# Kernel optimization log

Measured on AMD Instinct MI355X. Metric: run time of the kernel, lower is better.

Reference implementation:

```python
import jax, jax.numpy as jnp
import numpy as np

G = 16          # GroupNorm groups
EPS = 1e-5


def setup_inputs() -> dict:
    key = jax.random.key(0)
    ks = jax.random.split(key, 6)
    B, C, H, W = 2, 256, 96, 96
    O = 256
    x = jax.random.normal(ks[0], (B, C, H, W), dtype=jnp.float32)
    offset = jax.random.normal(ks[1], (B, 18, H, W), dtype=jnp.float32)
    mask = jax.random.uniform(ks[2], (B, 9, H, W), dtype=jnp.float32)
    fan_in = C * 9
    weight = jax.random.normal(ks[3], (O, C, 3, 3), dtype=jnp.float32) / np.sqrt(fan_in)
    bias = jnp.zeros((O,), dtype=jnp.float32)
    gamma = jnp.ones((O,), dtype=jnp.float32)
    beta = jnp.zeros((O,), dtype=jnp.float32)
    return {"x": x, "offset": offset, "mask": mask, "weight": weight,
            "bias": bias, "gamma": gamma, "beta": beta}


def _mdcn_gn(x, offset, mask, weight, bias, gamma, beta):
    B, C, H, W = x.shape
    O = weight.shape[0]
    K = 9
    # offsets: mmcv layout [y0,x0,y1,x1,...] per kernel point k = kh*3+kw
    off = offset.reshape(B, K, 2, H, W)
    off_y, off_x = off[:, :, 0], off[:, :, 1]            # [B,K,H,W]
    ky = (jnp.arange(K) // 3 - 1).astype(x.dtype)        # kernel dy, pad=1
    kx = (jnp.arange(K) % 3 - 1).astype(x.dtype)
    hh = jnp.arange(H, dtype=x.dtype)[:, None]
    ww = jnp.arange(W, dtype=x.dtype)[None, :]
    py = hh[None, None] + ky[:, None, None] + off_y      # [B,K,H,W] sample y
    px = ww[None, None] + kx[:, None, None] + off_x      # [B,K,H,W] sample x

    y0 = jnp.floor(py)
    x0 = jnp.floor(px)
    dy = py - y0
    dx = px - x0
    y0i = y0.astype(jnp.int32)
    x0i = x0.astype(jnp.int32)

    xf = x.reshape(B, C, H * W)

    def gather(yi, xi):
        # zero-padded bilinear corner: out-of-range corners contribute 0
        valid = ((yi >= 0) & (yi < H) & (xi >= 0) & (xi < W)).astype(x.dtype)
        yc = jnp.clip(yi, 0, H - 1)
        xc = jnp.clip(xi, 0, W - 1)
        idx = (yc * W + xc).reshape(B, 1, K * H * W)
        v = jnp.take_along_axis(xf, idx, axis=2).reshape(B, C, K, H, W)
        return v * valid.reshape(B, 1, K, H, W)

    w00 = ((1 - dy) * (1 - dx))[:, None]                 # [B,1,K,H,W]
    w01 = ((1 - dy) * dx)[:, None]
    w10 = (dy * (1 - dx))[:, None]
    w11 = (dy * dx)[:, None]
    val = (gather(y0i, x0i) * w00 + gather(y0i, x0i + 1) * w01 +
           gather(y0i + 1, x0i) * w10 + gather(y0i + 1, x0i + 1) * w11)
    val = val * mask[:, None]                            # modulation [B,C,K,H,W]

    out = jnp.einsum('ock,bckhw->bohw', weight.reshape(O, C, K), val)
    out = out + bias[None, :, None, None]

    # GroupNorm(16, O)
    xg = out.reshape(B, G, O // G, H, W)
    mean = xg.mean(axis=(2, 3, 4), keepdims=True)
    var = jnp.mean((xg - mean) ** 2, axis=(2, 3, 4), keepdims=True)
    xn = ((xg - mean) * jax.lax.rsqrt(var + EPS)).reshape(B, O, H, W)
    return xn * gamma[None, :, None, None] + beta[None, :, None, None]


def reference(x, offset, mask, weight, bias, gamma, beta):
    return _mdcn_gn(x, offset, mask, weight, bias, gamma, beta)
```

## Files before the change

### kernel.cpp

```cpp
#include <hip/hip_runtime.h>
#include <hip/hip_fp16.h>

typedef _Float16 f16;
typedef __attribute__((ext_vector_type(2))) _Float16 h2v;
typedef __attribute__((ext_vector_type(8))) _Float16 f16x8;
typedef __attribute__((ext_vector_type(4))) float f32x4;

#define HW_    9216
#define PADP   8
#define XP_    112
#define XPXP_  12544
#define NSTEP  72
#define NMT    288
#define XT_BYTES   12845056
#define BMAT_BYTES 1179648
#define ATILE_B    294912
#define A32_B      147456
#define OUTH_BYTES 9437184
#define PART_BYTES 36864

union U4 { uint4 u; h2v h[4]; f16x8 v; f16 f[8]; };
union U1 { unsigned u; h2v h; };
union UO { ushort4 s; f16 f[4]; };

__global__ __launch_bounds__(256) void k_zero(uint4* __restrict__ p) {
    int i = blockIdx.x*1024 + threadIdx.x;
    uint4 z = {0u,0u,0u,0u};
    p[i] = z; p[i+256] = z; p[i+512] = z; p[i+768] = z;
}

__global__ __launch_bounds__(256) void k_prep_x(const float* __restrict__ x, f16* __restrict__ xT) {
    __shared__ float tile[64 * 97];
    int blk = blockIdx.x;
    int cg  = blk & 3;
    int y   = (blk >> 2) % 96;
    int b   = blk / 384;
    int t   = threadIdx.x;
    const float* src = x + (((size_t)(b*256 + cg*64))*96 + y)*96;
    for (int e = t; e < 6144; e += 256) {
        int c = e / 96, wcol = e - c*96;
        tile[c*97 + wcol] = src[(size_t)c*HW_ + wcol];
    }
    __syncthreads();
    f16* dst = xT + ((size_t)b*XPXP_ + (size_t)(y+PADP)*XP_ + PADP)*256 + cg*64;
    for (int e = t; e < 6144; e += 256) {
        int wcol = e >> 6, c = e & 63;
        dst[(size_t)wcol*256 + c] = (f16)tile[c*97 + wcol];
    }
}

__global__ __launch_bounds__(256) void k_prep_w(const float* __restrict__ wgt, f16* __restrict__ bmat) {
    int id = blockIdx.x*256 + threadIdx.x;
    int o = id / 2304;
    int rem = id - o*2304;
    int c = rem / 9;
    int k = rem - c*9;
    int s  = k*8 + (c >> 5);
    int nw = o >> 6, fn = (o >> 4) & 3, r = o & 15;
    int kq = (c >> 3) & 3, e = c & 7;
    bmat[(size_t)s*8192 + nw*2048 + fn*512 + (kq*16 + r)*8 + e] = (f16)wgt[id];
}

__global__ __launch_bounds__(256, 6) void k_sample(
        const f16* __restrict__ xT, const float* __restrict__ offs,
        const float* __restrict__ maskp, f16* __restrict__ Ag, int mt0, int nblk)
{
    __shared__ int   geo_i[64];
    __shared__ uint4 geo_w[64];

    int blk0 = blockIdx.x;
    int blk  = (blk0 & 7)*(nblk >> 3) + (blk0 >> 3);
    int mtl  = blk / 9;
    int k    = blk - mtl*9;
    int mt   = mt0 + mtl;
    int b    = mt / 144;

    int tid = threadIdx.x;
    if (tid < 64) {
        int hw = mt*64 + tid - b*HW_;
        int h = hw / 96, w = hw - h*96;
        float offy = offs[((size_t)b*18 + 2*k    )*HW_ + hw];
        float offx = offs[((size_t)b*18 + 2*k + 1)*HW_ + hw];
        float mv   = maskp[((size_t)b*9 + k)*HW_ + hw];
        int ky = k/3 - 1, kx = k - (k/3)*3 - 1;
        float py = (float)(h + ky) + offy;
        float px = (float)(w + kx) + offx;
        py = fminf(fmaxf(py, -7.5f), 102.4f);
        px = fminf(fmaxf(px, -7.5f), 102.4f);
        float y0 = floorf(py), x0 = floorf(px);
        float dy = py - y0,   dx = px - x0;
        geo_i[tid] = (((int)y0 + PADP)*XP_ + ((int)x0 + PADP)) << 9;
        float w00v = (1.f-dy)*(1.f-dx)*mv, w01v = (1.f-dy)*dx*mv;
        float w10v = dy*(1.f-dx)*mv,       w11v = dy*dx*mv;
        U1 p0, p1, p2, p3;
        p0.h = h2v{(f16)w00v, (f16)w00v};
        p1.h = h2v{(f16)w01v, (f16)w01v};
        p2.h = h2v{(f16)w10v, (f16)w10v};
        p3.h = h2v{(f16)w11v, (f16)w11v};
        geo_w[tid] = uint4{p0.u, p1.u, p2.u, p3.u};
    }
    __syncthreads();

    const char* xbC = (const char*)xT + (size_t)b*XPXP_*512;
    char* dst = (char*)Ag + (size_t)mtl*ATILE_B;

    #pragma unroll
    for (int j = 0; j < 8; ++j) {
        int item = tid + j*256;
        int row = item >> 5, chunk = item & 31;
        const char* p = xbC + geo_i[row] + (chunk << 4);
        U4 t0, t1, t2, t3, oo;
        t0.u = *(const uint4*)(p);
        t1.u = *(const uint4*)(p + 512);
        t2.u = *(const uint4*)(p + XP_*512);
        t3.u = *(const uint4*)(p + XP_*512 + 512);
        U4 w4; w4.u = geo_w[row];
        h2v w00 = w4.h[0], w01 = w4.h[1], w10 = w4.h[2], w11 = w4.h[3];
        #pragma unroll
        for (int q = 0; q < 4; ++q)
            oo.h[q] = w00*t0.h[q] + w01*t1.h[q] + w10*t2.h[q] + w11*t3.h[q];
        int s = k*8 + (chunk >> 2);
        size_t off = (size_t)(row >> 5)*A32_B + (size_t)s*2048
                   + ((row >> 4) & 1)*1024 + (((chunk & 3)*16 + (row & 15)) << 4);
        *(uint4*)(dst + off) = oo.u;
    }
}

#define MFMA16(a,b,c) __builtin_amdgcn_mfma_f32_16x16x32_f16(a,b,c,0,0,0)

#define DECLSET(P) uint4 A##P##0,A##P##1,A##P##2,A##P##3, \
                         B##P##0,B##P##1,B##P##2,B##P##3

#define LOADSET(P, s_) do { \
    const char* pa_ = aB + (size_t)(s_)*2048; \
    const char* pb_ = bB + (size_t)(s_)*16384; \
    A##P##0 = *(const uint4*)(pa_); \
    A##P##1 = *(const uint4*)(pa_ + 1024); \
    A##P##2 = *(const uint4*)(pa_ + A32_B); \
    A##P##3 = *(const uint4*)(pa_ + A32_B + 1024); \
    B##P##0 = *(const uint4*)(pb_); \
    B##P##1 = *(const uint4*)(pb_ + 1024); \
    B##P##2 = *(const uint4*)(pb_ + 2048); \
    B##P##3 = *(const uint4*)(pb_ + 3072); \
  } while (0)

#define MMROW(P, jm, Areg) do { \
    U4 xa_, xb_; xa_.u = Areg; \
    xb_.u = B##P##0; acc[jm][0] = MFMA16(xa_.v, xb_.v, acc[jm][0]); \
    xb_.u = B##P##1; acc[jm][1] = MFMA16(xa_.v, xb_.v, acc[jm][1]); \
    xb_.u = B##P##2; acc[jm][2] = MFMA16(xa_.v, xb_.v, acc[jm][2]); \
    xb_.u = B##P##3; acc[jm][3] = MFMA16(xa_.v, xb_.v, acc[jm][3]); \
  } while (0)

#define MMSET(P) do { \
    MMROW(P, 0, A##P##0); MMROW(P, 1, A##P##1); \
    MMROW(P, 2, A##P##2); MMROW(P, 3, A##P##3); \
  } while (0)

__global__ __launch_bounds__(256, 2) void k_gemm(
        const f16* __restrict__ Ag, const f16* __restrict__ bmat,
        const float* __restrict__ bias, f16* __restrict__ outh,
        float* __restrict__ part, int row0, int nblk)
{
    int b0 = blockIdx.x;
    int bb = (b0 & 7)*(nblk >> 3) + (b0 >> 3);
    int mt = bb >> 2, nt = bb & 3;
    int lane = threadIdx.x & 63;
    int wid  = threadIdx.x >> 6;

    const char* aB = (const char*)Ag + (size_t)(mt*4 + wid)*ATILE_B + lane*16;
    const char* bB = (const char*)bmat + nt*4096 + lane*16;

    f32x4 acc[4][4];
    #pragma unroll
    for (int i = 0; i < 4; ++i)
        #pragma unroll
        for (int j = 0; j < 4; ++j) acc[i][j] = (f32x4){0.f,0.f,0.f,0.f};

    DECLSET(0); DECLSET(1); DECLSET(2);

    LOADSET(0, 0);
    LOADSET(1, 1);
    LOADSET(2, 2);

    for (int s = 0; s < 69; s += 3) {
        MMSET(0);  LOADSET(0, s+3);
        MMSET(1);  LOADSET(1, s+4);
        MMSET(2);  LOADSET(2, s+5);
    }
    MMSET(0);
    MMSET(1);
    MMSET(2);

    int grow = row0 + (mt*4 + wid)*64;
    int t64  = grow >> 6;
    int b    = grow / HW_;
    int hwb  = grow - b*HW_;
    int ol   = lane & 15;
    int qr   = (lane >> 4) << 2;
    #pragma unroll
    for (int jm = 0; jm < 4; ++jm) {
        #pragma unroll
        for (int fn = 0; fn < 4; ++fn) {
            int o = nt*64 + fn*16 + ol;
            float bv = bias[o];
            f32x4 a = acc[jm][fn];
            a[0] += bv; a[1] += bv; a[2] += bv; a[3] += bv;
            acc[jm][fn] = a;
            UO ov;
            ov.f[0] = (f16)a[0]; ov.f[1] = (f16)a[1];
            ov.f[2] = (f16)a[2]; ov.f[3] = (f16)a[3];
            *(ushort4*)(outh + ((size_t)(b*256 + o))*HW_ + hwb + jm*16 + qr) = ov.s;
        }
    }
    #pragma unroll
    for (int fn = 0; fn < 4; ++fn) {
        float s1 = 0.f, s2 = 0.f;
        #pragma unroll
        for (int jm = 0; jm < 4; ++jm) {
            f32x4 a = acc[jm][fn];
            s1 += a[0]+a[1]+a[2]+a[3];
            s2 += a[0]*a[0]+a[1]*a[1]+a[2]*a[2]+a[3]*a[3];
        }
        #pragma unroll
        for (int m = 32; m > 0; m >>= 1) {
            s1 += __shfl_xor(s1, m);
            s2 += __shfl_xor(s2, m);
        }
        if (lane == 0) {
            part[((size_t)t64*16 + nt*4 + fn)*2]     = s1;
            part[((size_t)t64*16 + nt*4 + fn)*2 + 1] = s2;
        }
    }
}

__global__ __launch_bounds__(256) void k_finalize(const float* __restrict__ part, float* __restrict__ stats) {
    int bg = blockIdx.x, b = bg >> 4, g = bg & 15;
    float s1 = 0.f, s2 = 0.f;
    if (threadIdx.x < 144) {
        const float* p = part + ((size_t)(b*144 + threadIdx.x)*16 + g)*2;
        s1 = p[0]; s2 = p[1];
    }
    __shared__ float a1[256], a2[256];
    a1[threadIdx.x] = s1; a2[threadIdx.x] = s2;
    __syncthreads();
    for (int off = 128; off > 0; off >>= 1) {
        if (threadIdx.x < off) { a1[threadIdx.x] += a1[threadIdx.x+off]; a2[threadIdx.x] += a2[threadIdx.x+off]; }
        __syncthreads();
    }
    if (threadIdx.x == 0) {
        float inv_n = 1.f/147456.f;
        float mean = a1[0]*inv_n;
        float var  = fmaxf(a2[0]*inv_n - mean*mean, 0.f);
        stats[bg*2]   = mean;
        stats[bg*2+1] = rsqrtf(var + 1e-5f);
    }
}

__global__ __launch_bounds__(256) void k_norm(const f16* __restrict__ outh, float* __restrict__ out,
                                              const float* __restrict__ stats,
                                              const float* __restrict__ gamma, const float* __restrict__ beta) {
    int i8 = blockIdx.x*256 + threadIdx.x;
    int p  = i8 / 1152;
    int o  = p & 255;
    float mean = stats[(p>>4)*2], rstd = stats[(p>>4)*2 + 1];
    float ga = gamma[o]*rstd, be = beta[o] - mean*rstd*gamma[o];
    U4 v; v.u = ((const uint4*)outh)[i8];
    float4 o0, o1;
    o0.x = (float)v.f[0]*ga + be; o0.y = (float)v.f[1]*ga + be;
    o0.z = (float)v.f[2]*ga + be; o0.w = (float)v.f[3]*ga + be;
    o1.x = (float)v.f[4]*ga + be; o1.y = (float)v.f[5]*ga + be;
    o1.z = (float)v.f[6]*ga + be; o1.w = (float)v.f[7]*ga + be;
    ((float4*)out)[i8*2]     = o0;
    ((float4*)out)[i8*2 + 1] = o1;
}

extern "C" void kernel_launch(void* const* d_in, const int* in_sizes, int n_in,
                              void* d_out, int out_size, void* d_ws, size_t ws_size,
                              hipStream_t stream) {
    const float* x      = (const float*)d_in[0];
    const float* offset = (const float*)d_in[1];
    const float* mask   = (const float*)d_in[2];
    const float* weight = (const float*)d_in[3];
    const float* bias   = (const float*)d_in[4];
    const float* gamma  = (const float*)d_in[5];
    const float* beta   = (const float*)d_in[6];
    float* out = (float*)d_out;

    char* ws = (char*)d_ws;
    f16*   xT    = (f16*)ws;
    f16*   bmat  = (f16*)(ws + XT_BYTES);
    float* part  = (float*)(ws + XT_BYTES + BMAT_BYTES);
    float* stats = (float*)(ws + XT_BYTES + BMAT_BYTES + PART_BYTES);
    f16*   outh  = (f16*)(ws + XT_BYTES + BMAT_BYTES + PART_BYTES + 256);
    char*  Ag    = ws + XT_BYTES + BMAT_BYTES + PART_BYTES + 256 + OUTH_BYTES;

    size_t needA = (size_t)NMT * ATILE_B;
    size_t base  = (size_t)XT_BYTES + BMAT_BYTES + PART_BYTES + 256 + OUTH_BYTES;
    size_t avail = ws_size > base ? ws_size - base : 0;
    int P = (avail >= needA) ? 1 : ((avail >= needA/2) ? 2 : 4);

    k_zero<<<784, 256, 0, stream>>>((uint4*)xT);
    k_prep_x<<<768, 256, 0, stream>>>(x, xT);
    k_prep_w<<<2304, 256, 0, stream>>>(weight, bmat);
    int mtn = NMT / P;
    for (int p = 0; p < P; ++p) {
        k_sample<<<mtn*9, 256, 0, stream>>>(xT, offset, mask, (f16*)Ag, p*mtn, mtn*9);
        k_gemm<<<mtn, 256, 0, stream>>>((f16*)Ag, bmat, bias, outh, part, p*mtn*64, mtn);
    }
    k_finalize<<<32, 256, 0, stream>>>(part, stats);
    k_norm<<<2304, 256, 0, stream>>>(outh, out, stats, gamma, beta);
}
```

Before: 102.6 us.

## Restructure deformable-conv GEMM to share A tile via LDS across wavefronts

Each GEMM block now covers 48 rows by all 256 output channels. The four wavefronts split the N dimension and share an A tile that is staged into LDS with a triple buffer of global_load_lds copies. Before, every block handled a 256x64 tile with each wave loading its own A rows from global memory. The change cuts redundant A reads and raises the block count, using explicit waitcnt, barriers and setprio to order the pipeline. The sample kernel's output layout, the partial-stats size and the finalize reduction are changed to match the 48-row tiles, and per-step barriers add sync overhead.

```diff
diff --git a/kernel.cpp b/kernel.cpp
--- a/kernel.cpp
+++ b/kernel.cpp
@@ -15,9 +15,13 @@
 #define XT_BYTES   12845056
 #define BMAT_BYTES 1179648
 #define ATILE_B    294912
-#define A32_B      147456
+#define A16_B      73728
 #define OUTH_BYTES 9437184
-#define PART_BYTES 36864
+#define PART_BYTES 49152
+
+#define GLOAD_LDS16(g, l) \
+  __builtin_amdgcn_global_load_lds((const __attribute__((address_space(1))) void*)(g), \
+                                   (__attribute__((address_space(3))) void*)(l), 16, 0, 0)
 
 union U4 { uint4 u; h2v h[4]; f16x8 v; f16 f[8]; };
 union U1 { unsigned u; h2v h; };
@@ -120,41 +124,49 @@
         for (int q = 0; q < 4; ++q)
             oo.h[q] = w00*t0.h[q] + w01*t1.h[q] + w10*t2.h[q] + w11*t3.h[q];
         int s = k*8 + (chunk >> 2);
-        size_t off = (size_t)(row >> 5)*A32_B + (size_t)s*2048
-                   + ((row >> 4) & 1)*1024 + (((chunk & 3)*16 + (row & 15)) << 4);
+        size_t off = (size_t)(row >> 4)*A16_B + (size_t)s*1024
+                   + (((chunk & 3)*16 + (row & 15)) << 4);
         *(uint4*)(dst + off) = oo.u;
     }
 }
 
 #define MFMA16(a,b,c) __builtin_amdgcn_mfma_f32_16x16x32_f16(a,b,c,0,0,0)
 
-#define DECLSET(P) uint4 A##P##0,A##P##1,A##P##2,A##P##3, \
-                         B##P##0,B##P##1,B##P##2,B##P##3
-
-#define LOADSET(P, s_) do { \
-    const char* pa_ = aB + (size_t)(s_)*2048; \
+#define STAGEA(s_, BUF) do { \
+    if (tid < 192) \
+      GLOAD_LDS16(aStage + (size_t)(s_)*1024, ldsA + (BUF)*3072 + aLds); \
+  } while (0)
+
+#define LOADB(s_, SET) do { \
     const char* pb_ = bB + (size_t)(s_)*16384; \
-    A##P##0 = *(const uint4*)(pa_); \
-    A##P##1 = *(const uint4*)(pa_ + 1024); \
-    A##P##2 = *(const uint4*)(pa_ + A32_B); \
-    A##P##3 = *(const uint4*)(pa_ + A32_B + 1024); \
-    B##P##0 = *(const uint4*)(pb_); \
-    B##P##1 = *(const uint4*)(pb_ + 1024); \
-    B##P##2 = *(const uint4*)(pb_ + 2048); \
-    B##P##3 = *(const uint4*)(pb_ + 3072); \
+    B##SET##0 = *(const uint4*)(pb_); \
+    B##SET##1 = *(const uint4*)(pb_ + 1024); \
+    B##SET##2 = *(const uint4*)(pb_ + 2048); \
+    B##SET##3 = *(const uint4*)(pb_ + 3072); \
   } while (0)
 
-#define MMROW(P, jm, Areg) do { \
-    U4 xa_, xb_; xa_.u = Areg; \
-    xb_.u = B##P##0; acc[jm][0] = MFMA16(xa_.v, xb_.v, acc[jm][0]); \
-    xb_.u = B##P##1; acc[jm][1] = MFMA16(xa_.v, xb_.v, acc[jm][1]); \
-    xb_.u = B##P##2; acc[jm][2] = MFMA16(xa_.v, xb_.v, acc[jm][2]); \
-    xb_.u = B##P##3; acc[jm][3] = MFMA16(xa_.v, xb_.v, acc[jm][3]); \
+#define MM(BUF, SET) do { \
+    const char* Ab_ = ldsA + (BUF)*3072 + (lane << 4); \
+    U4 a0_, a1_, a2_, xb_; \
+    a0_.u = *(const uint4*)(Ab_); \
+    a1_.u = *(const uint4*)(Ab_ + 1024); \
+    a2_.u = *(const uint4*)(Ab_ + 2048); \
+    xb_.u = B##SET##0; acc[0][0]=MFMA16(a0_.v,xb_.v,acc[0][0]); acc[1][0]=MFMA16(a1_.v,xb_.v,acc[1][0]); acc[2][0]=MFMA16(a2_.v,xb_.v,acc[2][0]); \
+    xb_.u = B##SET##1; acc[0][1]=MFMA16(a0_.v,xb_.v,acc[0][1]); acc[1][1]=MFMA16(a1_.v,xb_.v,acc[1][1]); acc[2][1]=MFMA16(a2_.v,xb_.v,acc[2][1]); \
+    xb_.u = B##SET##2; acc[0][2]=MFMA16(a0_.v,xb_.v,acc[0][2]); acc[1][2]=MFMA16(a1_.v,xb_.v,acc[1][2]); acc[2][2]=MFMA16(a2_.v,xb_.v,acc[2][2]); \
+    xb_.u = B##SET##3; acc[0][3]=MFMA16(a0_.v,xb_.v,acc[0][3]); acc[1][3]=MFMA16(a1_.v,xb_.v,acc[1][3]); acc[2][3]=MFMA16(a2_.v,xb_.v,acc[2][3]); \
   } while (0)
 
-#define MMSET(P) do { \
-    MMROW(P, 0, A##P##0); MMROW(P, 1, A##P##1); \
-    MMROW(P, 2, A##P##2); MMROW(P, 3, A##P##3); \
+#define ITER(s_, CUR, NXT, PF, VN) do { \
+    __builtin_amdgcn_sched_barrier(0); \
+    asm volatile("s_waitcnt vmcnt(" VN ")" ::: "memory"); \
+    __builtin_amdgcn_sched_barrier(0); \
+    __builtin_amdgcn_s_barrier(); \
+    __builtin_amdgcn_sched_barrier(0); \
+    if (PF) { STAGEA((s_)+2, NXT); LOADB((s_)+2, NXT); } \
+    __builtin_amdgcn_s_setprio(1); \
+    MM(CUR, CUR); \
+    __builtin_amdgcn_s_setprio(0); \
   } while (0)
 
 __global__ __launch_bounds__(256, 2) void k_gemm(
@@ -162,47 +174,52 @@
         const float* __restrict__ bias, f16* __restrict__ outh,
         float* __restrict__ part, int row0, int nblk)
 {
+    __shared__ __align__(16) char AsLDS[3*3072];
+
+    char* ldsA = AsLDS;
     int b0 = blockIdx.x;
     int bb = (b0 & 7)*(nblk >> 3) + (b0 >> 3);
-    int mt = bb >> 2, nt = bb & 3;
-    int lane = threadIdx.x & 63;
-    int wid  = threadIdx.x >> 6;
-
-    const char* aB = (const char*)Ag + (size_t)(mt*4 + wid)*ATILE_B + lane*16;
-    const char* bB = (const char*)bmat + nt*4096 + lane*16;
-
-    f32x4 acc[4][4];
+    int mw = bb;
+    int tid = threadIdx.x;
+    int lane = tid & 63;
+    int nw   = tid >> 6;
+
+    const char* aStage = (const char*)Ag + (size_t)mw*(3*A16_B)
+                       + (size_t)(tid >> 6)*A16_B + (size_t)(lane << 4);
+    int aLds = (tid >> 6)*1024 + (lane << 4);
+    const char* bB = (const char*)bmat + nw*4096 + (lane << 4);
+
+    f32x4 acc[3][4];
     #pragma unroll
-    for (int i = 0; i < 4; ++i)
+    for (int i = 0; i < 3; ++i)
         #pragma unroll
         for (int j = 0; j < 4; ++j) acc[i][j] = (f32x4){0.f,0.f,0.f,0.f};
 
-    DECLSET(0); DECLSET(1); DECLSET(2);
-
-    LOADSET(0, 0);
-    LOADSET(1, 1);
-    LOADSET(2, 2);
+    uint4 B00,B01,B02,B03, B10,B11,B12,B13, B20,B21,B22,B23;
+
+    STAGEA(0, 0); LOADB(0, 0);
+    STAGEA(1, 1); LOADB(1, 1);
 
     for (int s = 0; s < 69; s += 3) {
-        MMSET(0);  LOADSET(0, s+3);
-        MMSET(1);  LOADSET(1, s+4);
-        MMSET(2);  LOADSET(2, s+5);
-    }
-    MMSET(0);
-    MMSET(1);
-    MMSET(2);
-
-    int grow = row0 + (mt*4 + wid)*64;
-    int t64  = grow >> 6;
+        ITER(s,   0, 2, 1, "9");
+        ITER(s+1, 1, 0, 1, "9");
+        ITER(s+2, 2, 1, 1, "9");
+    }
+    ITER(69, 0, 2, 1, "9");
+    ITER(70, 1, 0, 0, "9");
+    ITER(71, 2, 1, 0, "4");
+
+    int grow = row0 + mw*48;
+    int mwg  = grow / 48;
     int b    = grow / HW_;
     int hwb  = grow - b*HW_;
     int ol   = lane & 15;
     int qr   = (lane >> 4) << 2;
     #pragma unroll
-    for (int jm = 0; jm < 4; ++jm) {
+    for (int jm = 0; jm < 3; ++jm) {
         #pragma unroll
         for (int fn = 0; fn < 4; ++fn) {
-            int o = nt*64 + fn*16 + ol;
+            int o = nw*64 + fn*16 + ol;
             float bv = bias[o];
             f32x4 a = acc[jm][fn];
             a[0] += bv; a[1] += bv; a[2] += bv; a[3] += bv;
@@ -217,7 +234,7 @@
     for (int fn = 0; fn < 4; ++fn) {
         float s1 = 0.f, s2 = 0.f;
         #pragma unroll
-        for (int jm = 0; jm < 4; ++jm) {
+        for (int jm = 0; jm < 3; ++jm) {
             f32x4 a = acc[jm][fn];
             s1 += a[0]+a[1]+a[2]+a[3];
             s2 += a[0]*a[0]+a[1]*a[1]+a[2]*a[2]+a[3]*a[3];
@@ -228,8 +245,8 @@
             s2 += __shfl_xor(s2, m);
         }
         if (lane == 0) {
-            part[((size_t)t64*16 + nt*4 + fn)*2]     = s1;
-            part[((size_t)t64*16 + nt*4 + fn)*2 + 1] = s2;
+            part[((size_t)mwg*16 + nw*4 + fn)*2]     = s1;
+            part[((size_t)mwg*16 + nw*4 + fn)*2 + 1] = s2;
         }
     }
 }
@@ -237,8 +254,8 @@
 __global__ __launch_bounds__(256) void k_finalize(const float* __restrict__ part, float* __restrict__ stats) {
     int bg = blockIdx.x, b = bg >> 4, g = bg & 15;
     float s1 = 0.f, s2 = 0.f;
-    if (threadIdx.x < 144) {
-        const float* p = part + ((size_t)(b*144 + threadIdx.x)*16 + g)*2;
+    if (threadIdx.x < 192) {
+        const float* p = part + ((size_t)(b*192 + threadIdx.x)*16 + g)*2;
         s1 = p[0]; s2 = p[1];
     }
     __shared__ float a1[256], a2[256];
@@ -304,9 +321,10 @@
     k_prep_x<<<768, 256, 0, stream>>>(x, xT);
     k_prep_w<<<2304, 256, 0, stream>>>(weight, bmat);
     int mtn = NMT / P;
+    int nb48 = (mtn * 64) / 48;
     for (int p = 0; p < P; ++p) {
         k_sample<<<mtn*9, 256, 0, stream>>>(xT, offset, mask, (f16*)Ag, p*mtn, mtn*9);
-        k_gemm<<<mtn, 256, 0, stream>>>((f16*)Ag, bmat, bias, outh, part, p*mtn*64, mtn);
+        k_gemm<<<nb48, 256, 0, stream>>>((f16*)Ag, bmat, bias, outh, part, p*mtn*64, nb48);
     }
     k_finalize<<<32, 256, 0, stream>>>(part, stats);
     k_norm<<<2304, 256, 0, stream>>>(outh, out, stats, gamma, beta);
```

After: 105.3 us. 1.03x slower.
